# Kernel optimization log

Measured on AMD Instinct MI355X. Metric: run time of the kernel, lower is better.

## Reference

```python
import jax, jax.numpy as jnp
import numpy as np

B, K, D = 65536, 1024, 256
COMMITMENT_COST = 0.25


def setup_inputs() -> dict:
    key = jax.random.key(0)
    kz, kw = jax.random.split(key)
    z = jax.random.normal(kz, (B, D), dtype=jnp.float32)
    # torch init: uniform_(-1/num_embeddings, 1/num_embeddings)
    weight = jax.random.uniform(kw, (K, D), dtype=jnp.float32,
                                minval=-1.0 / K, maxval=1.0 / K)
    return {"z": z, "weight": weight}


def reference(z, weight):
    # squared L2 distances via expansion: ||z||^2 - 2 z.e + ||e||^2  -> [B, K]
    dists = (jnp.sum(z * z, axis=1, keepdims=True)
             - 2.0 * (z @ weight.T)
             + jnp.sum(weight * weight, axis=1))
    indices = jnp.argmin(dists, axis=1)          # [B]
    z_q = weight[indices]                         # [B, D] gather

    sg_z = jax.lax.stop_gradient(z)
    mse = jnp.mean((z_q - sg_z) ** 2)
    commitment_loss = COMMITMENT_COST * mse      # F.mse_loss(z.detach(), z_q)
    vq_loss = mse + commitment_loss              # F.mse_loss(z_q, z.detach()) + commitment

    # straight-through estimator
    z_q_st = z + jax.lax.stop_gradient(z_q - z)
    return z_q_st, vq_loss, indices
```

## Files before the change

### kernel.cpp

```cpp
#include <hip/hip_runtime.h>
#include <math.h>

#define B_N 65536
#define K_N 1024
#define D_N 256
#define CAPW 512
#define NWV 8

typedef __attribute__((ext_vector_type(8))) short bf16x8;
typedef __attribute__((ext_vector_type(4))) float f32x4;

__device__ __forceinline__ unsigned short f2bf(float f) {
    unsigned u = __float_as_uint(f);
    return (unsigned short)((u + 0x7FFFu + ((u >> 16) & 1u)) >> 16);
}
__device__ __forceinline__ unsigned encf(float f) {
    unsigned u = __float_as_uint(f);
    return u ^ ((unsigned)((int)u >> 31) | 0x80000000u);
}
__device__ __forceinline__ float decf(unsigned e) {
    unsigned u = (e & 0x80000000u) ? (e ^ 0x80000000u) : ~e;
    return __uint_as_float(u);
}
__device__ __forceinline__ void gload_lds16(const void* g, void* l) {
    __builtin_amdgcn_global_load_lds(
        (const __attribute__((address_space(1))) unsigned int*)g,
        (__attribute__((address_space(3))) unsigned int*)l, 16, 0, 0);
}

__device__ __forceinline__ float chain_dot(const float* __restrict__ zp,
                                           const float* __restrict__ wp) {
    float acc = 0.0f;
    #pragma unroll 1
    for (int j = 0; j < 64; ++j) {
        float4 za = *reinterpret_cast<const float4*>(zp + (j << 2));
        float4 wa = *reinterpret_cast<const float4*>(wp + (j << 2));
        acc = fmaf(za.x, wa.x, acc);
        acc = fmaf(za.y, wa.y, acc);
        acc = fmaf(za.z, wa.z, acc);
        acc = fmaf(za.w, wa.w, acc);
    }
    return acc;
}

__device__ __forceinline__ int pA(int i, int k) {
    return ((i + k) & 15) - 7 + 9 * ((k >> 4) & 1);
}
__device__ __forceinline__ int pB(int j, int k) {
    return ((j + 3 * k) & 15) - 7 + 5 * ((k >> 4) & 1);
}

__global__ void mfma_probe_kernel(int* __restrict__ flag) {
    const int l = threadIdx.x & 63;
    const int c15 = l & 15, g = l >> 4;
    bf16x8 afr[8], bfr[8];
    #pragma unroll
    for (int m = 0; m < 8; ++m)
        #pragma unroll
        for (int e = 0; e < 8; ++e) {
            const int k = m * 32 + g * 8 + e;
            afr[m][e] = (short)f2bf((float)pA(c15, k));
            bfr[m][e] = (short)f2bf((float)pB(c15, k));
        }
    f32x4 acc = {0.f, 0.f, 0.f, 0.f};
    #pragma unroll
    for (int m = 0; m < 8; ++m)
        acc = __builtin_amdgcn_mfma_f32_16x16x32_bf16(afr[m], bfr[m], acc, 0, 0, 0);
    int h1 = 1, h2 = 1;
    #pragma unroll 1
    for (int reg = 0; reg < 4; ++reg) {
        const int q = 4 * g + reg;
        int e1 = 0, e2 = 0;
        for (int k = 0; k < 32; ++k) {
            e1 += pA(q, k) * pB(c15, k);
            e2 += pA(c15, k) * pB(q, k);
        }
        e1 *= 8; e2 *= 8;
        if (acc[reg] != (float)e1) h1 = 0;
        if (acc[reg] != (float)e2) h2 = 0;
    }
    h1 = __all(h1); h2 = __all(h2);
    if (threadIdx.x == 0) *flag = h1 ? 0 : (h2 ? 1 : 2);
}

__global__ void wprep_kernel(const float* __restrict__ w,
                             float* __restrict__ ww,
                             unsigned short* __restrict__ wb) {
    int wave = (int)((blockIdx.x * blockDim.x + threadIdx.x) >> 6);
    int lane = threadIdx.x & 63;
    if (wave >= K_N) return;
    const float4 v = *reinterpret_cast<const float4*>(w + ((size_t)wave << 8) + (lane << 2));
    float s = v.x * v.x + v.y * v.y + v.z * v.z + v.w * v.w;
    #pragma unroll
    for (int off = 32; off; off >>= 1) s += __shfl_xor(s, off, 64);
    if (lane == 0) ww[wave] = s;
    ushort4 b;
    b.x = f2bf(v.x); b.y = f2bf(v.y); b.z = f2bf(v.z); b.w = f2bf(v.w);
    const int mp = lane >> 3;
    const int gp = (lane >> 1) & 3;
    const int hp = (wave >> 4) & 1;
    const size_t off_b = (size_t)(wave >> 5) * 16384
        + (size_t)(((hp * 8 + mp) * 64 + gp * 16 + (wave & 15)) * 16)
        + (size_t)((lane & 1) * 8);
    *reinterpret_cast<ushort4*>((char*)wb + off_b) = b;
}

__global__ __launch_bounds__(512, 4)
void vq_mfma_kernel(const float* __restrict__ z, const float* __restrict__ w,
                    const unsigned short* __restrict__ wb,
                    const float* __restrict__ ww,
                    const int* __restrict__ flagp,
                    float* __restrict__ zq_out,
                    float* __restrict__ idxf_out,
                    double* __restrict__ partial) {
    __shared__ alignas(16) short wbl[3][8192];
    __shared__ float wwlds[1024];
    __shared__ unsigned short rc[NWV][CAPW];
    __shared__ unsigned short dqv[NWV][CAPW];
    __shared__ float zz_l[NWV][16], band_l[NWV][16], thrm[NWV][16];
    __shared__ unsigned rowminU[NWV][16];
    __shared__ unsigned long long bestk[NWV][16];

    const int tid = threadIdx.x;
    const int wv = tid >> 6, l = tid & 63;
    const int c15 = l & 15, g = l >> 4;
    const int b0 = blockIdx.x << 7;
    const int rbase = b0 + (wv << 4);
    const int flag = flagp[0];
    const bool fb0 = !(flag == 0 || flag == 1);

#define STAGE(T, BUF) do {                                                    \
        const char* _s = (const char*)wb + (size_t)(T) * 16384 + tid * 16;    \
        char* _d = (char*)&wbl[BUF][0] + tid * 16;                            \
        gload_lds16(_s,         _d);                                          \
        gload_lds16(_s + 8192,  _d + 8192);                                   \
    } while (0)

    STAGE(0, 0);

    if (l < 16) {
        rowminU[wv][l] = 0xFFFFFFFFu;
        bestk[wv][l]   = ~0ull;
    }
    reinterpret_cast<float2*>(wwlds)[tid] = reinterpret_cast<const float2*>(ww)[tid];

    #pragma unroll 1
    for (int half = 0; half < 2; ++half) {
        float4 vrow[8];
        #pragma unroll
        for (int r = 0; r < 8; ++r)
            vrow[r] = *reinterpret_cast<const float4*>(
                z + ((size_t)(rbase + half * 8 + r) << 8) + (l << 2));
        #pragma unroll
        for (int r = 0; r < 8; ++r) {
            const float4 v = vrow[r];
            float s = v.x * v.x + v.y * v.y + v.z * v.z + v.w * v.w;
            float a = fabsf(v.x) + fabsf(v.y) + fabsf(v.z) + fabsf(v.w);
            #pragma unroll
            for (int off = 32; off; off >>= 1) {
                s += __shfl_xor(s, off, 64);
                a += __shfl_xor(a, off, 64);
            }
            if (l == 0) {
                zz_l[wv][half * 8 + r]   = s;
                band_l[wv][half * 8 + r] = a * 2.0e-5f + 1.0e-3f;
            }
        }
    }

    STAGE(1, 1);

    bool fbw = fb0;
    int n = 0;

    int ml[4], cl[4];
    #pragma unroll
    for (int reg = 0; reg < 4; ++reg) {
        if (flag == 1) { ml[reg] = c15;          cl[reg] = 4 * g + reg; }
        else           { ml[reg] = 4 * g + reg;  cl[reg] = c15;         }
    }

    bf16x8 afr[8];
    {
        const float* zr = z + ((size_t)(rbase + c15) << 8) + (g << 3);
        #pragma unroll
        for (int m = 0; m < 8; ++m) {
            float4 lo = *reinterpret_cast<const float4*>(zr + (m << 5));
            float4 hi = *reinterpret_cast<const float4*>(zr + (m << 5) + 4);
            bf16x8 f;
            f[0] = (short)f2bf(lo.x); f[1] = (short)f2bf(lo.y);
            f[2] = (short)f2bf(lo.z); f[3] = (short)f2bf(lo.w);
            f[4] = (short)f2bf(hi.x); f[5] = (short)f2bf(hi.y);
            f[6] = (short)f2bf(hi.z); f[7] = (short)f2bf(hi.w);
            afr[m] = f;
        }
    }

    __syncthreads();

    float zzv[4], bdv[4];
    #pragma unroll
    for (int reg = 0; reg < 4; ++reg) {
        zzv[reg] = zz_l[wv][ml[reg]];
        bdv[reg] = band_l[wv][ml[reg]];
    }

    float runmin[4] = {INFINITY, INFINITY, INFINITY, INFINITY};
    int base = 0;

    if (!fb0) {
        #pragma unroll 1
        for (int t = 0; t <= 32; ++t) {
            if (t + 2 <= 32) {
                const int st = (t + 2 <= 31) ? (t + 2) : 0;
                STAGE(st, (t + 2) % 3);
            }

            const short* sb = wbl[t % 3];
            const int tc = (t <= 31) ? t : 0;
            #pragma unroll
            for (int h = 0; h < 2; ++h) {
                f32x4 acc = {0.f, 0.f, 0.f, 0.f};
                #pragma unroll
                for (int m = 0; m < 8; ++m) {
                    bf16x8 bfr = *reinterpret_cast<const bf16x8*>(
                        &sb[((h * 8 + m) << 9) + (l << 3)]);
                    acc = __builtin_amdgcn_mfma_f32_16x16x32_bf16(afr[m], bfr, acc, 0, 0, 0);
                }
                #pragma unroll
                for (int reg = 0; reg < 4; ++reg) {
                    const int code = (tc << 5) + (h << 4) + cl[reg];
                    const float dist = (zzv[reg] - 2.0f * acc[reg]) + wwlds[code];
                    if (t > 0) {
                        const bool pred = (dist <= runmin[reg] + bdv[reg]);
                        const unsigned long long mask = __ballot(pred);
                        if (pred) {
                            const int slot = base + (int)__popcll(mask & ((1ull << l) - 1ull));
                            if (slot < CAPW) {
                                rc[wv][slot] = (unsigned short)((ml[reg] << 10) | code);
                                union { _Float16 h16; unsigned short u; } cv;
                                cv.h16 = (_Float16)(dist - zzv[reg]);
                                dqv[wv][slot] = cv.u;
                            }
                        }
                        base += (int)__popcll(mask);
                    }
                    if (t < 32) runmin[reg] = fminf(runmin[reg], dist);
                }
            }

            if (t < 32) {
                if (flag == 1) {
                    #pragma unroll
                    for (int reg = 0; reg < 4; ++reg) {
                        runmin[reg] = fminf(runmin[reg], __shfl_xor(runmin[reg], 16, 64));
                        runmin[reg] = fminf(runmin[reg], __shfl_xor(runmin[reg], 32, 64));
                    }
                } else {
                    #pragma unroll
                    for (int reg = 0; reg < 4; ++reg) {
                        runmin[reg] = fminf(runmin[reg], __shfl_xor(runmin[reg], 1, 64));
                        runmin[reg] = fminf(runmin[reg], __shfl_xor(runmin[reg], 2, 64));
                        runmin[reg] = fminf(runmin[reg], __shfl_xor(runmin[reg], 4, 64));
                        runmin[reg] = fminf(runmin[reg], __shfl_xor(runmin[reg], 8, 64));
                    }
                }
                if (t + 2 <= 32) {
                    asm volatile("s_waitcnt vmcnt(2) lgkmcnt(0)" ::: "memory");
                } else {
                    asm volatile("s_waitcnt vmcnt(0) lgkmcnt(0)" ::: "memory");
                }
                __builtin_amdgcn_sched_barrier(0);
                __builtin_amdgcn_s_barrier();
                __builtin_amdgcn_sched_barrier(0);
            }
        }

        n = base;
        if (n > CAPW) fbw = true;

        #pragma unroll
        for (int reg = 0; reg < 4; ++reg)
            atomicMin(&rowminU[wv][ml[reg]], encf(runmin[reg]));
        if (l < 16)
            thrm[wv][l] = (decf(rowminU[wv][l]) + band_l[wv][l]) - zz_l[wv][l] + 4.0e-4f;
    }
#undef STAGE

    if (!fbw) {
        int viol = 0;
        #pragma unroll 1
        for (int i = l; i < n; i += 64) {
            const int e = rc[wv][i];
            const int m = e >> 10, code = e & 1023;
            union { _Float16 h16; unsigned short u; } cv;
            cv.u = dqv[wv][i];
            const float dval = (float)cv.h16;
            if (dval <= thrm[wv][m]) {
                const float dot = chain_dot(z + ((size_t)(rbase + m) << 8),
                                            w + ((size_t)code << 8));
                const float dist = (zz_l[wv][m] - 2.0f * dot) + wwlds[code];
                if (fabsf((dval + zz_l[wv][m]) - dist) > band_l[wv][m] + 4.0e-4f)
                    viol = 1;
                atomicMin(&bestk[wv][m],
                          ((unsigned long long)encf(dist) << 32) | (unsigned)code);
            }
        }
        if (__any(viol)) fbw = true;
    }
    if (fbw) {
        #pragma unroll 1
        for (int m = 0; m < 16; ++m) {
            const float zzm = zz_l[wv][m];
            const float* zp = z + ((size_t)(rbase + m) << 8);
            for (int code = l; code < 1024; code += 64) {
                const float dist = (zzm - 2.0f * chain_dot(zp, w + ((size_t)code << 8)))
                                 + wwlds[code];
                atomicMin(&bestk[wv][m],
                          ((unsigned long long)encf(dist) << 32) | (unsigned)code);
            }
        }
    }

    if (l < 16) {
        const int code = (int)(unsigned)(bestk[wv][l] & 0xFFFFFFFFull);
        idxf_out[rbase + l] = (float)code;
    }

    int codes[16];
    #pragma unroll
    for (int rr = 0; rr < 16; ++rr)
        codes[rr] = (int)(unsigned)(bestk[wv][rr] & 0xFFFFFFFFull);
    double s = 0.0;
    #pragma unroll 2
    for (int rr = 0; rr < 16; ++rr) {
        const int code = codes[rr];
        const float4 wv4 = *reinterpret_cast<const float4*>(
            w + ((size_t)code << 8) + (l << 2));
        const float4 zv4 = *reinterpret_cast<const float4*>(
            z + ((size_t)(rbase + rr) << 8) + (l << 2));
        *reinterpret_cast<float4*>(
            zq_out + ((size_t)(rbase + rr) << 8) + (l << 2)) = wv4;
        const float dx = wv4.x - zv4.x, dy = wv4.y - zv4.y;
        const float dz = wv4.z - zv4.z, dw = wv4.w - zv4.w;
        s += (double)dx * dx + (double)dy * dy + (double)dz * dz + (double)dw * dw;
    }
    __syncthreads();
    double* sd = reinterpret_cast<double*>(&wbl[0][0]);
    sd[tid] = s;
    __syncthreads();
    #pragma unroll
    for (int off = 256; off; off >>= 1) {
        if (tid < off) sd[tid] += sd[tid + off];
        __syncthreads();
    }
    if (tid == 0) partial[blockIdx.x] = sd[0];
}

__global__ void finalize_loss_kernel(const double* __restrict__ partial,
                                     float* __restrict__ out) {
    __shared__ double sd[256];
    const int t = threadIdx.x;
    double s = 0.0;
    for (int i = t; i < 512; i += 256) s += partial[i];
    sd[t] = s;
    __syncthreads();
    #pragma unroll
    for (int off = 128; off; off >>= 1) {
        if (t < off) sd[t] += sd[t + off];
        __syncthreads();
    }
    if (t == 0) {
        double mse = sd[0] / ((double)B_N * (double)D_N);
        out[0] = (float)(mse * 1.25);
    }
}

extern "C" void kernel_launch(void* const* d_in, const int* in_sizes, int n_in,
                              void* d_out, int out_size, void* d_ws, size_t ws_size,
                              hipStream_t stream) {
    const float* z = (const float*)d_in[0];
    const float* w = (const float*)d_in[1];

    float* out  = (float*)d_out;
    float* zq   = out;
    float* loss = out + (size_t)B_N * D_N;
    float* idxf = loss + 1;

    char* wsb = (char*)d_ws;
    float*          ww      = (float*)(wsb);
    unsigned short* wb      = (unsigned short*)(wsb + 4096);
    int*            flag    = (int*)(wsb + 528384);
    double*         partial = (double*)(wsb + 528448);

    mfma_probe_kernel<<<1, 64, 0, stream>>>(flag);

    wprep_kernel<<<K_N / 4, 256, 0, stream>>>(w, ww, wb);

    vq_mfma_kernel<<<B_N / 128, 512, 0, stream>>>(z, w, wb, ww, flag,
                                                  zq, idxf, partial);

    finalize_loss_kernel<<<1, 256, 0, stream>>>(partial, loss);
}
```

Before: 178.5 us.

## Software-pipeline MFMA tiles with epilogue processing of the previous tile

Restructures the main codebook loop so that each iteration issues the MFMAs for tile C into one pair of accumulators while running the distance, ballot and candidate-collection epilogue on tile C-1's accumulators. The loop is manually unrolled by two with ping-pong accumulator sets. The aim is to hide MFMA latency behind the scalar and ballot work and to let the two 16-column halves run as independent MFMA chains. It also skips the popcount and store path when a ballot mask is empty. The cost is more live accumulator registers and more complicated iteration-boundary conditions.

Result: no change. 179.4 us (+0.5%).

```diff
diff --git a/kernel.cpp b/kernel.cpp
--- a/kernel.cpp
+++ b/kernel.cpp
@@ -208,72 +208,92 @@
     float runmin[4] = {INFINITY, INFINITY, INFINITY, INFINITY};
     int base = 0;
 
+#define ITER(C, CUR0, CUR1, PRV0, PRV1) do {                                  \
+    if ((C) <= 32) {                                                          \
+        if ((C) <= 30) {                                                      \
+            const int _st = ((C) + 2 <= 31) ? ((C) + 2) : 0;                  \
+            STAGE(_st, ((C) + 2) % 3);                                        \
+        }                                                                     \
+        const short* _sb = wbl[(C) % 3];                                      \
+        CUR0 = (f32x4){0.f, 0.f, 0.f, 0.f};                                   \
+        CUR1 = (f32x4){0.f, 0.f, 0.f, 0.f};                                   \
+        _Pragma("unroll")                                                     \
+        for (int m = 0; m < 8; ++m) {                                         \
+            bf16x8 _b = *reinterpret_cast<const bf16x8*>(                     \
+                &_sb[(m << 9) + (l << 3)]);                                   \
+            CUR0 = __builtin_amdgcn_mfma_f32_16x16x32_bf16(afr[m], _b, CUR0, 0, 0, 0); \
+        }                                                                     \
+        _Pragma("unroll")                                                     \
+        for (int m = 0; m < 8; ++m) {                                         \
+            bf16x8 _b = *reinterpret_cast<const bf16x8*>(                     \
+                &_sb[((8 + m) << 9) + (l << 3)]);                             \
+            CUR1 = __builtin_amdgcn_mfma_f32_16x16x32_bf16(afr[m], _b, CUR1, 0, 0, 0); \
+        }                                                                     \
+    }                                                                         \
+    if ((C) >= 1) {                                                           \
+        const int _tc = ((C) <= 32) ? ((C) - 1) : 0;                          \
+        const bool _docol = ((C) >= 2);                                       \
+        const bool _dofm = ((C) <= 32);                                       \
+        _Pragma("unroll")                                                     \
+        for (int h = 0; h < 2; ++h) {                                         \
+            const f32x4 _acc = h ? (PRV1) : (PRV0);                           \
+            _Pragma("unroll")                                                 \
+            for (int reg = 0; reg < 4; ++reg) {                               \
+                const int _code = (_tc << 5) + (h << 4) + cl[reg];            \
+                const float _dist = (zzv[reg] - 2.0f * _acc[reg]) + wwlds[_code]; \
+                if (_docol) {                                                 \
+                    const bool _pred = (_dist <= runmin[reg] + bdv[reg]);     \
+                    const unsigned long long _mask = __ballot(_pred);         \
+                    if (_mask) {                                              \
+                        if (_pred) {                                          \
+                            const int _slot = base + (int)__popcll(_mask & ((1ull << l) - 1ull)); \
+                            if (_slot < CAPW) {                               \
+                                rc[wv][_slot] = (unsigned short)((ml[reg] << 10) | _code); \
+                                union { _Float16 h16; unsigned short u; } _cv; \
+                                _cv.h16 = (_Float16)(_dist - zzv[reg]);       \
+                                dqv[wv][_slot] = _cv.u;                       \
+                            }                                                 \
+                        }                                                     \
+                        base += (int)__popcll(_mask);                         \
+                    }                                                         \
+                }                                                             \
+                if (_dofm) runmin[reg] = fminf(runmin[reg], _dist);           \
+            }                                                                 \
+        }                                                                     \
+        if (_dofm) {                                                          \
+            if (flag == 1) {                                                  \
+                _Pragma("unroll")                                             \
+                for (int reg = 0; reg < 4; ++reg) {                           \
+                    runmin[reg] = fminf(runmin[reg], __shfl_xor(runmin[reg], 16, 64)); \
+                    runmin[reg] = fminf(runmin[reg], __shfl_xor(runmin[reg], 32, 64)); \
+                }                                                             \
+            } else {                                                          \
+                _Pragma("unroll")                                             \
+                for (int reg = 0; reg < 4; ++reg) {                           \
+                    runmin[reg] = fminf(runmin[reg], __shfl_xor(runmin[reg], 1, 64)); \
+                    runmin[reg] = fminf(runmin[reg], __shfl_xor(runmin[reg], 2, 64)); \
+                    runmin[reg] = fminf(runmin[reg], __shfl_xor(runmin[reg], 4, 64)); \
+                    runmin[reg] = fminf(runmin[reg], __shfl_xor(runmin[reg], 8, 64)); \
+                }                                                             \
+            }                                                                 \
+        }                                                                     \
+    }                                                                         \
+    if ((C) <= 31) {                                                          \
+        if ((C) <= 30) { asm volatile("s_waitcnt vmcnt(2) lgkmcnt(0)" ::: "memory"); } \
+        else           { asm volatile("s_waitcnt vmcnt(0) lgkmcnt(0)" ::: "memory"); } \
+        __builtin_amdgcn_sched_barrier(0);                                    \
+        __builtin_amdgcn_s_barrier();                                         \
+        __builtin_amdgcn_sched_barrier(0);                                    \
+    }                                                                         \
+} while (0)
+
     if (!fb0) {
+        f32x4 aA0 = {0.f, 0.f, 0.f, 0.f}, aA1 = {0.f, 0.f, 0.f, 0.f};
+        f32x4 aB0 = {0.f, 0.f, 0.f, 0.f}, aB1 = {0.f, 0.f, 0.f, 0.f};
         #pragma unroll 1
-        for (int t = 0; t <= 32; ++t) {
-            if (t + 2 <= 32) {
-                const int st = (t + 2 <= 31) ? (t + 2) : 0;
-                STAGE(st, (t + 2) % 3);
-            }
-
-            const short* sb = wbl[t % 3];
-            const int tc = (t <= 31) ? t : 0;
-            #pragma unroll
-            for (int h = 0; h < 2; ++h) {
-                f32x4 acc = {0.f, 0.f, 0.f, 0.f};
-                #pragma unroll
-                for (int m = 0; m < 8; ++m) {
-                    bf16x8 bfr = *reinterpret_cast<const bf16x8*>(
-                        &sb[((h * 8 + m) << 9) + (l << 3)]);
-                    acc = __builtin_amdgcn_mfma_f32_16x16x32_bf16(afr[m], bfr, acc, 0, 0, 0);
-                }
-                #pragma unroll
-                for (int reg = 0; reg < 4; ++reg) {
-                    const int code = (tc << 5) + (h << 4) + cl[reg];
-                    const float dist = (zzv[reg] - 2.0f * acc[reg]) + wwlds[code];
-                    if (t > 0) {
-                        const bool pred = (dist <= runmin[reg] + bdv[reg]);
-                        const unsigned long long mask = __ballot(pred);
-                        if (pred) {
-                            const int slot = base + (int)__popcll(mask & ((1ull << l) - 1ull));
-                            if (slot < CAPW) {
-                                rc[wv][slot] = (unsigned short)((ml[reg] << 10) | code);
-                                union { _Float16 h16; unsigned short u; } cv;
-                                cv.h16 = (_Float16)(dist - zzv[reg]);
-                                dqv[wv][slot] = cv.u;
-                            }
-                        }
-                        base += (int)__popcll(mask);
-                    }
-                    if (t < 32) runmin[reg] = fminf(runmin[reg], dist);
-                }
-            }
-
-            if (t < 32) {
-                if (flag == 1) {
-                    #pragma unroll
-                    for (int reg = 0; reg < 4; ++reg) {
-                        runmin[reg] = fminf(runmin[reg], __shfl_xor(runmin[reg], 16, 64));
-                        runmin[reg] = fminf(runmin[reg], __shfl_xor(runmin[reg], 32, 64));
-                    }
-                } else {
-                    #pragma unroll
-                    for (int reg = 0; reg < 4; ++reg) {
-                        runmin[reg] = fminf(runmin[reg], __shfl_xor(runmin[reg], 1, 64));
-                        runmin[reg] = fminf(runmin[reg], __shfl_xor(runmin[reg], 2, 64));
-                        runmin[reg] = fminf(runmin[reg], __shfl_xor(runmin[reg], 4, 64));
-                        runmin[reg] = fminf(runmin[reg], __shfl_xor(runmin[reg], 8, 64));
-                    }
-                }
-                if (t + 2 <= 32) {
-                    asm volatile("s_waitcnt vmcnt(2) lgkmcnt(0)" ::: "memory");
-                } else {
-                    asm volatile("s_waitcnt vmcnt(0) lgkmcnt(0)" ::: "memory");
-                }
-                __builtin_amdgcn_sched_barrier(0);
-                __builtin_amdgcn_s_barrier();
-                __builtin_amdgcn_sched_barrier(0);
-            }
+        for (int c = 0; c < 34; c += 2) {
+            ITER(c,     aA0, aA1, aB0, aB1);
+            ITER(c + 1, aB0, aB1, aA0, aA1);
         }
 
         n = base;
@@ -285,6 +305,7 @@
         if (l < 16)
             thrm[wv][l] = (decf(rowminU[wv][l]) + band_l[wv][l]) - zz_l[wv][l] + 4.0e-4f;
     }
+#undef ITER
 #undef STAGE
 
     if (!fbw) {
```
